# Optimization experiments

Hardware: AMD Instinct MI355X
Metric: run time of the kernel (lower is better)

The kernel has to match this reference:

```python
import jax, jax.numpy as jnp
import numpy as np


def setup_inputs() -> dict:
    key = jax.random.key(0)
    ks = jax.random.split(key, 6)
    B, La, Lb = 32, 2048, 2048
    return {
        "a": jax.random.normal(ks[0], (B, La), dtype=jnp.float32),
        "b": jax.random.normal(ks[1], (B, Lb), dtype=jnp.float32),
        "in_proj_w": jax.random.normal(ks[2], (3, 1), dtype=jnp.float32),
        "in_proj_b": jax.random.normal(ks[3], (3,), dtype=jnp.float32) * 0.1,
        "out_w": jax.random.normal(ks[4], (1, 1), dtype=jnp.float32),
        "out_b": jax.random.normal(ks[5], (1,), dtype=jnp.float32) * 0.1,
    }


def reference(a, b, in_proj_w, in_proj_b, out_w, out_b):
    # embed_dim=1, num_heads=1 MHA degenerates to scalar affine projections.
    wq, wk, wv = in_proj_w[0, 0], in_proj_w[1, 0], in_proj_w[2, 0]
    bq, bk, bv = in_proj_b[0], in_proj_b[1], in_proj_b[2]
    q = a * wq + bq                      # [B, La]
    k = b * wk + bk                      # [B, Lb]
    v = b * wv + bv                      # [B, Lb]
    # scale = 1/sqrt(head_dim=1) = 1; scores via outer product per batch
    scores = q[:, :, None] * k[:, None, :]        # [B, La, Lb]
    attn = jax.nn.softmax(scores, axis=-1)        # [B, La, Lb]
    ctx = jnp.einsum("bqk,bk->bq", attn, v)       # [B, La]
    x = ctx * out_w[0, 0] + out_b[0]              # out_proj (1x1)
    # residual with a_f, then exact (erf) GELU as in F.gelu default
    return jax.nn.gelu(x + a, approximate=False)[..., None]  # [B, La, 1]
```

## Files before the change

kernel.cpp:

```cpp
#include <hip/hip_runtime.h>
#include <math.h>


#define BATCH 32
#define LA 2048
#define LB 2048
#define SPLIT 16
#define MI 4
#define CHUNK (LB / SPLIT)
#define P2 (CHUNK / 2)
#define CP (P2 + 1)
#define THREADS 256
#define IPB ((THREADS / SPLIT) * MI)
#define BLOCKS_PER_B (LA / IPB)

__global__ __launch_bounds__(THREADS, 4)
void cross_attn_kernel(const float* __restrict__ a,
                       const float* __restrict__ b,
                       const float* __restrict__ w_in,
                       const float* __restrict__ b_in,
                       const float* __restrict__ w_out,
                       const float* __restrict__ b_out,
                       float* __restrict__ out)
{
    __shared__ float4 kv[SPLIT * CP];
    __shared__ float red[8];

    const int tid = threadIdx.x;
    const int bb  = blockIdx.x / BLOCKS_PER_B;
    const int cc  = blockIdx.x % BLOCKS_PER_B;

    const float wq = w_in[0], wk = w_in[1], wv = w_in[2];
    const float bq = b_in[0], bk = b_in[1], bv = b_in[2];
    const float ow = w_out[0], ob = b_out[0];

    const float* brow = b + (size_t)bb * LB;
    float kmaxl = -INFINITY, kminl = INFINITY;
    {
        const int j0 = tid * 8;
        float4 b0 = *(const float4*)(brow + j0);
        float4 b1 = *(const float4*)(brow + j0 + 4);
        float bv8[8] = {b0.x, b0.y, b0.z, b0.w, b1.x, b1.y, b1.z, b1.w};
        const int c  = j0 >> 7;
        const int pi = (j0 & (CHUNK - 1)) >> 1;
        float4* dst = &kv[c * CP + pi];
        #pragma unroll
        for (int e = 0; e < 4; ++e) {
            float k0 = fmaf(bv8[2 * e],     wk, bk);
            float v0 = fmaf(bv8[2 * e],     wv, bv);
            float k1 = fmaf(bv8[2 * e + 1], wk, bk);
            float v1 = fmaf(bv8[2 * e + 1], wv, bv);
            dst[e] = make_float4(k0, v0, k1, v1);
            kmaxl = fmaxf(kmaxl, fmaxf(k0, k1));
            kminl = fminf(kminl, fminf(k0, k1));
        }
    }

    #pragma unroll
    for (int off = 1; off < 64; off <<= 1) {
        kmaxl = fmaxf(kmaxl, __shfl_xor(kmaxl, off, 64));
        kminl = fminf(kminl, __shfl_xor(kminl, off, 64));
    }
    const int lane = tid & 63, wave = tid >> 6;
    if (lane == 0) { red[wave] = kmaxl; red[4 + wave] = kminl; }
    __syncthreads();
    const float kmax = fmaxf(fmaxf(red[0], red[1]), fmaxf(red[2], red[3]));
    const float kmin = fminf(fminf(red[4], red[5]), fminf(red[6], red[7]));

    const int split = tid & (SPLIT - 1);
    const int g     = tid >> 4;
    const int i0    = cc * IPB + g * MI;
    const float4 av = *(const float4*)(a + (size_t)bb * LA + i0);
    const float avals[MI] = {av.x, av.y, av.z, av.w};

    const float L2E = 1.4426950408889634f;
    float t2[MI], nm2[MI], num[MI], den[MI];
    #pragma unroll
    for (int m = 0; m < MI; ++m) {
        float t = fmaf(avals[m], wq, bq);
        t2[m]  = t * L2E;
        nm2[m] = -((t2[m] >= 0.0f) ? t2[m] * kmax : t2[m] * kmin);
        num[m] = 0.0f;
        den[m] = 0.0f;
    }

    const float4* kvp = &kv[split * CP];

    #pragma unroll 8
    for (int p = 0; p < P2; ++p) {
        const float4 q = kvp[p];
        #pragma unroll
        for (int m = 0; m < MI; ++m) {
            float e0 = __builtin_amdgcn_exp2f(fmaf(t2[m], q.x, nm2[m]));
            num[m] = fmaf(e0, q.y, num[m]);
            den[m] += e0;
            float e1 = __builtin_amdgcn_exp2f(fmaf(t2[m], q.z, nm2[m]));
            num[m] = fmaf(e1, q.w, num[m]);
            den[m] += e1;
        }
    }

    #pragma unroll
    for (int mask = 1; mask < SPLIT; mask <<= 1) {
        #pragma unroll
        for (int m = 0; m < MI; ++m) {
            num[m] += __shfl_xor(num[m], mask, 64);
            den[m] += __shfl_xor(den[m], mask, 64);
        }
    }

    if (split == 0) {
        float4 res;
        float* rp = &res.x;
        #pragma unroll
        for (int m = 0; m < MI; ++m) {
            float ctx = num[m] / den[m];
            float x   = fmaf(ctx, ow, ob);
            float y   = x + avals[m];
            rp[m] = 0.5f * y * (1.0f + erff(y * 0.70710678118654752f));
        }
        *(float4*)(out + (size_t)bb * LA + i0) = res;
    }
}

extern "C" void kernel_launch(void* const* d_in, const int* in_sizes, int n_in,
                              void* d_out, int out_size, void* d_ws, size_t ws_size,
                              hipStream_t stream) {
    const float* a  = (const float*)d_in[0];
    const float* b  = (const float*)d_in[1];
    const float* wi = (const float*)d_in[2];
    const float* bi = (const float*)d_in[3];
    const float* wo = (const float*)d_in[4];
    const float* bo = (const float*)d_in[5];
    float* out = (float*)d_out;

    dim3 grid(BATCH * BLOCKS_PER_B);
    dim3 block(THREADS);
    cross_attn_kernel<<<grid, block, 0, stream>>>(a, b, wi, bi, wo, bo, out);
}
```

Before: 83.96 us.

## Use packed fp32 FMA math, wider per-thread query tile, and interleaved KV layout

Each thread now handles 8 queries instead of 4, and the key split across lanes goes from 16 to 32. The shared KV buffer is changed from a padded per-split layout to one interleaved by split, so lanes read consecutive float4s. The FMA and accumulation math is rewritten with 2-wide float vectors so the compiler can emit packed fp32 instructions (v_pk_fma_f32); exp2 stays scalar. The aim is more ALU throughput per LDS load and fewer LDS bank conflicts, at the cost of higher register pressure and a longer shuffle reduction.

```diff
diff --git a/kernel.cpp b/kernel.cpp
--- a/kernel.cpp
+++ b/kernel.cpp
@@ -5,14 +5,16 @@
 #define BATCH 32
 #define LA 2048
 #define LB 2048
-#define SPLIT 16
-#define MI 4
+#define SPLIT 32
+#define MI 8
 #define CHUNK (LB / SPLIT)
 #define P2 (CHUNK / 2)
-#define CP (P2 + 1)
 #define THREADS 256
-#define IPB ((THREADS / SPLIT) * MI)
+#define GROUPS (THREADS / SPLIT)
+#define IPB (GROUPS * MI)
 #define BLOCKS_PER_B (LA / IPB)
+
+typedef float v2f __attribute__((ext_vector_type(2)));
 
 __global__ __launch_bounds__(THREADS, 4)
 void cross_attn_kernel(const float* __restrict__ a,
@@ -23,7 +25,7 @@
                        const float* __restrict__ b_out,
                        float* __restrict__ out)
 {
-    __shared__ float4 kv[SPLIT * CP];
+    __shared__ float4 kv2[P2 * SPLIT];
     __shared__ float red[8];
 
     const int tid = threadIdx.x;
@@ -41,16 +43,15 @@
         float4 b0 = *(const float4*)(brow + j0);
         float4 b1 = *(const float4*)(brow + j0 + 4);
         float bv8[8] = {b0.x, b0.y, b0.z, b0.w, b1.x, b1.y, b1.z, b1.w};
-        const int c  = j0 >> 7;
-        const int pi = (j0 & (CHUNK - 1)) >> 1;
-        float4* dst = &kv[c * CP + pi];
+        const int c  = j0 >> 6;
+        const int p0 = (j0 & (CHUNK - 1)) >> 1;
         #pragma unroll
         for (int e = 0; e < 4; ++e) {
             float k0 = fmaf(bv8[2 * e],     wk, bk);
             float v0 = fmaf(bv8[2 * e],     wv, bv);
             float k1 = fmaf(bv8[2 * e + 1], wk, bk);
             float v1 = fmaf(bv8[2 * e + 1], wv, bv);
-            dst[e] = make_float4(k0, v0, k1, v1);
+            kv2[(p0 + e) * SPLIT + c] = make_float4(k0, v0, k1, v1);
             kmaxl = fmaxf(kmaxl, fmaxf(k0, k1));
             kminl = fminf(kminl, fminf(k0, k1));
         }
@@ -68,58 +69,77 @@
     const float kmin = fminf(fminf(red[4], red[5]), fminf(red[6], red[7]));
 
     const int split = tid & (SPLIT - 1);
-    const int g     = tid >> 4;
+    const int g     = tid >> 5;
     const int i0    = cc * IPB + g * MI;
-    const float4 av = *(const float4*)(a + (size_t)bb * LA + i0);
-    const float avals[MI] = {av.x, av.y, av.z, av.w};
+    const float* ap = a + (size_t)bb * LA + i0;
+    float4 a0 = *(const float4*)(ap);
+    float4 a1 = *(const float4*)(ap + 4);
+    const float avals[MI] = {a0.x, a0.y, a0.z, a0.w, a1.x, a1.y, a1.z, a1.w};
 
     const float L2E = 1.4426950408889634f;
-    float t2[MI], nm2[MI], num[MI], den[MI];
+    v2f t2v[MI / 2], nm2v[MI / 2], numv[MI / 2], denv[MI / 2];
     #pragma unroll
-    for (int m = 0; m < MI; ++m) {
-        float t = fmaf(avals[m], wq, bq);
-        t2[m]  = t * L2E;
-        nm2[m] = -((t2[m] >= 0.0f) ? t2[m] * kmax : t2[m] * kmin);
-        num[m] = 0.0f;
-        den[m] = 0.0f;
+    for (int m = 0; m < MI / 2; ++m) {
+        #pragma unroll
+        for (int h = 0; h < 2; ++h) {
+            float t  = fmaf(avals[2 * m + h], wq, bq);
+            float t2 = t * L2E;
+            t2v[m][h]  = t2;
+            nm2v[m][h] = -((t2 >= 0.0f) ? t2 * kmax : t2 * kmin);
+        }
+        numv[m] = (v2f)(0.0f);
+        denv[m] = (v2f)(0.0f);
     }
 
-    const float4* kvp = &kv[split * CP];
+    const float4* kvp = kv2 + split;
 
     #pragma unroll 8
     for (int p = 0; p < P2; ++p) {
-        const float4 q = kvp[p];
+        const float4 q = kvp[p * SPLIT];
+        const v2f k0 = (v2f)(q.x), v0 = (v2f)(q.y);
+        const v2f k1 = (v2f)(q.z), v1 = (v2f)(q.w);
         #pragma unroll
-        for (int m = 0; m < MI; ++m) {
-            float e0 = __builtin_amdgcn_exp2f(fmaf(t2[m], q.x, nm2[m]));
-            num[m] = fmaf(e0, q.y, num[m]);
-            den[m] += e0;
-            float e1 = __builtin_amdgcn_exp2f(fmaf(t2[m], q.z, nm2[m]));
-            num[m] = fmaf(e1, q.w, num[m]);
-            den[m] += e1;
+        for (int m = 0; m < MI / 2; ++m) {
+            v2f a0v = __builtin_elementwise_fma(t2v[m], k0, nm2v[m]);
+            v2f e0;
+            e0.x = __builtin_amdgcn_exp2f(a0v.x);
+            e0.y = __builtin_amdgcn_exp2f(a0v.y);
+            numv[m] = __builtin_elementwise_fma(e0, v0, numv[m]);
+            denv[m] += e0;
+            v2f a1v = __builtin_elementwise_fma(t2v[m], k1, nm2v[m]);
+            v2f e1;
+            e1.x = __builtin_amdgcn_exp2f(a1v.x);
+            e1.y = __builtin_amdgcn_exp2f(a1v.y);
+            numv[m] = __builtin_elementwise_fma(e1, v1, numv[m]);
+            denv[m] += e1;
         }
     }
 
     #pragma unroll
     for (int mask = 1; mask < SPLIT; mask <<= 1) {
         #pragma unroll
-        for (int m = 0; m < MI; ++m) {
-            num[m] += __shfl_xor(num[m], mask, 64);
-            den[m] += __shfl_xor(den[m], mask, 64);
+        for (int m = 0; m < MI / 2; ++m) {
+            numv[m].x += __shfl_xor(numv[m].x, mask, 64);
+            numv[m].y += __shfl_xor(numv[m].y, mask, 64);
+            denv[m].x += __shfl_xor(denv[m].x, mask, 64);
+            denv[m].y += __shfl_xor(denv[m].y, mask, 64);
         }
     }
 
     if (split == 0) {
-        float4 res;
-        float* rp = &res.x;
+        float res[MI];
         #pragma unroll
         for (int m = 0; m < MI; ++m) {
-            float ctx = num[m] / den[m];
+            float nm  = (m & 1) ? numv[m >> 1].y : numv[m >> 1].x;
+            float dn  = (m & 1) ? denv[m >> 1].y : denv[m >> 1].x;
+            float ctx = nm / dn;
             float x   = fmaf(ctx, ow, ob);
             float y   = x + avals[m];
-            rp[m] = 0.5f * y * (1.0f + erff(y * 0.70710678118654752f));
+            res[m] = 0.5f * y * (1.0f + erff(y * 0.70710678118654752f));
         }
-        *(float4*)(out + (size_t)bb * LA + i0) = res;
+        float* op = out + (size_t)bb * LA + i0;
+        *(float4*)(op)     = make_float4(res[0], res[1], res[2], res[3]);
+        *(float4*)(op + 4) = make_float4(res[4], res[5], res[6], res[7]);
     }
 }
 
```

Result: no change. 85.34 us (+1.6%).
